# Optimization experiments

Hardware: AMD Instinct MI355X
Metric: run time of the kernel (lower is better)

The kernel has to match this reference:

```python
import jax, jax.numpy as jnp
import numpy as np

N_NODES = 50000
N_EDGES = 500000
D = 256  # node_dim = edge_dim = out_dim; in_dim = 2*D


def setup_inputs() -> dict:
    key = jax.random.key(0)
    ks = jax.random.split(key, 9)
    x = jax.random.normal(ks[0], (N_NODES, D), dtype=jnp.float32)
    edge_index = jax.random.randint(ks[1], (2, N_EDGES), 0, N_NODES, dtype=jnp.int64)
    edge_attr = jax.random.normal(ks[2], (N_EDGES, D), dtype=jnp.float32)
    u = jax.random.normal(ks[3], (1, D), dtype=jnp.float32)
    batch = jnp.zeros((N_NODES,), dtype=jnp.int64)
    scale = 1.0 / np.sqrt(2 * D)
    W1 = jax.random.normal(ks[4], (2 * D, D), dtype=jnp.float32) * scale
    b1 = jax.random.normal(ks[5], (D,), dtype=jnp.float32) * scale
    W2 = jax.random.normal(ks[6], (2 * D, D), dtype=jnp.float32) * scale
    b2 = jax.random.normal(ks[7], (D,), dtype=jnp.float32) * scale
    return {"x": x, "edge_index": edge_index, "edge_attr": edge_attr, "u": u,
            "batch": batch, "W1": W1, "b1": b1, "W2": W2, "b2": b2}


def reference(x, edge_index, edge_attr, u, batch, W1, b1, W2, b2):
    row, col = edge_index[0], edge_index[1]
    # gather source-node features and concat with edge features: [E, 2D]
    h = jnp.concatenate([x[row], edge_attr], axis=1)
    h = jax.nn.relu(h @ W1 + b1)  # node_mlp_1
    # scatter-mean over destination nodes
    agg = jax.ops.segment_sum(h, col, num_segments=N_NODES)
    cnt = jax.ops.segment_sum(jnp.ones((h.shape[0],), h.dtype), col, num_segments=N_NODES)
    agg = agg / jnp.maximum(cnt, 1.0)[:, None]
    out = jnp.concatenate([x, agg], axis=1)  # [N, 2D]
    return jax.nn.relu(out @ W2 + b2)  # node_mlp_2
```

## Files before the change

### kernel.cpp

```cpp
#include <hip/hip_runtime.h>

#define N_NODES 50000
#define N_EDGES 500000
#define D 256
#define TWO_D 512

typedef __attribute__((ext_vector_type(8))) __bf16 bf16x8;
typedef __attribute__((ext_vector_type(4))) float f32x4;
typedef unsigned short ushort_t;

__device__ __forceinline__ unsigned short f2bf(float f) {
    unsigned int u = __builtin_bit_cast(unsigned int, f);
    u += 0x7FFFu + ((u >> 16) & 1u);
    return (unsigned short)(u >> 16);
}
__device__ __forceinline__ unsigned int pk2(float lo, float hi) {
    return (unsigned int)f2bf(lo) | ((unsigned int)f2bf(hi) << 16);
}

__device__ __forceinline__ void barrier_nodrain() {
    asm volatile("s_waitcnt lgkmcnt(0)" ::: "memory");
    __builtin_amdgcn_s_barrier();
    __builtin_amdgcn_sched_barrier(0);
}


__global__ void k_zero(float* __restrict__ p, int n4) {
    int i = blockIdx.x * blockDim.x + threadIdx.x;
    if (i < n4) ((float4*)p)[i] = make_float4(0.f, 0.f, 0.f, 0.f);
}

__global__ void k_cvt_x(const float* __restrict__ x, ushort_t* __restrict__ xb, int n8) {
    int i = blockIdx.x * blockDim.x + threadIdx.x;
    if (i < n8) {
        const float4* s = (const float4*)(x + (size_t)i * 8);
        float4 a = s[0], b = s[1];
        uint4 o;
        o.x = pk2(a.x, a.y); o.y = pk2(a.z, a.w);
        o.z = pk2(b.x, b.y); o.w = pk2(b.z, b.w);
        *(uint4*)(xb + (size_t)i * 8) = o;
    }
}

__global__ void k_wt(const float* __restrict__ w, ushort_t* __restrict__ wt, int KW) {
    int n = blockIdx.x;
    for (int k = threadIdx.x; k < KW; k += blockDim.x)
        wt[(size_t)n * KW + k] = f2bf(w[(size_t)k * D + n]);
}

__global__ void k_count_i(const int* __restrict__ coli, int* __restrict__ cnt) {
    int e = blockIdx.x * blockDim.x + threadIdx.x;
    if (e < N_EDGES) atomicAdd(&cnt[coli[e]], 1);
}


__device__ __forceinline__ int iscan_block(int v, int tid) {
    int lane = tid & 63, wv = tid >> 6;
    int s = v;
    #pragma unroll
    for (int off = 1; off < 64; off <<= 1) {
        int t = __shfl_up(s, off, 64);
        if (lane >= off) s += t;
    }
    __shared__ int wsum[4];
    if (lane == 63) wsum[wv] = s;
    __syncthreads();
    #pragma unroll
    for (int w = 0; w < 3; ++w)
        if (wv > w) s += wsum[w];
    return s;
}

__global__ void k_scan_a(const int* __restrict__ cnt, int* __restrict__ rowptr,
                         int* __restrict__ bsum) {
    int i = blockIdx.x * 256 + threadIdx.x;
    int v = (i < N_NODES) ? cnt[i] : 0;
    int s = iscan_block(v, threadIdx.x);
    if (i < N_NODES) rowptr[i] = s - v;
    if (threadIdx.x == 255) bsum[blockIdx.x] = s;
}

__global__ void k_scan_b(int* __restrict__ bsum, int nb) {
    int i = threadIdx.x;
    int v = (i < nb) ? bsum[i] : 0;
    int s = iscan_block(v, i);
    if (i < nb) bsum[i] = s - v;
}

__global__ void k_scan_c(int* __restrict__ rowptr, const int* __restrict__ bsum,
                         int* __restrict__ cursor) {
    int i = blockIdx.x * 256 + threadIdx.x;
    if (i < N_NODES) {
        int r = rowptr[i] + bsum[blockIdx.x];
        rowptr[i] = r;
        cursor[i] = r;
    }
    if (i == 0) rowptr[N_NODES] = N_EDGES;
}

__global__ void k_fill(const int* __restrict__ coli, const int* __restrict__ rowi,
                       const int* __restrict__ rowptr, int* __restrict__ cursor,
                       int* __restrict__ elist, int* __restrict__ rowg,
                       int* __restrict__ posnode) {
    int e = blockIdx.x * blockDim.x + threadIdx.x;
    if (e < N_EDGES) {
        const int c = coli[e];
        const int p = atomicAdd(&cursor[c], 1);
        elist[p] = e;
        rowg[p] = rowi[e];
        const int t0 = p & ~63;
        const int inter = (rowptr[c] >= t0) && (rowptr[c + 1] <= t0 + 64);
        posnode[p] = (c << 1) | inter;
    }
}

__global__ __launch_bounds__(256) void k_xw1(
    const ushort_t* __restrict__ xb, const ushort_t* __restrict__ w1at,
    const float* __restrict__ b1, float* __restrict__ xw1)
{
    __shared__ __align__(16) ushort_t As[64 * 64];
    __shared__ __align__(16) ushort_t Bs[256 * 64];
    const int tid = threadIdx.x;
    const int wave = tid >> 6, lane = tid & 63;
    const int lr = lane & 15, lh = lane >> 4;
    const int n0 = blockIdx.x * 64;

    const int sm = tid >> 2;
    const int sc = (tid & 3) << 4;
    int ns = n0 + sm; if (ns >= N_NODES) ns = N_NODES - 1;
    const ushort_t* xrow = xb + (size_t)ns * D;
    const ushort_t* wrow = w1at + (size_t)tid * D;
    const int swA = (sm & 7) << 3;
    const int swB = (tid & 7) << 3;

    f32x4 acc[4][4];
    #pragma unroll
    for (int i = 0; i < 4; ++i)
        #pragma unroll
        for (int j = 0; j < 4; ++j)
            acc[i][j] = (f32x4){0.f, 0.f, 0.f, 0.f};

    for (int kk = 0; kk < 4; ++kk) {
        const int k0 = kk << 6;
        const uint4* sx = (const uint4*)(xrow + k0 + sc);
        uint4 av0 = sx[0], av1 = sx[1];
        const uint4* wsv = (const uint4*)(wrow + k0);
        uint4 w0 = wsv[0], w1 = wsv[1], w2 = wsv[2], w3 = wsv[3];
        uint4 w4 = wsv[4], w5 = wsv[5], w6 = wsv[6], w7 = wsv[7];

        __syncthreads();
        *(uint4*)&As[sm * 64 + ( sc      ^ swA)] = av0;
        *(uint4*)&As[sm * 64 + ((sc + 8) ^ swA)] = av1;
        {
            const int base = tid * 64;
            *(uint4*)&Bs[base + ( 0 ^ swB)] = w0;
            *(uint4*)&Bs[base + ( 8 ^ swB)] = w1;
            *(uint4*)&Bs[base + (16 ^ swB)] = w2;
            *(uint4*)&Bs[base + (24 ^ swB)] = w3;
            *(uint4*)&Bs[base + (32 ^ swB)] = w4;
            *(uint4*)&Bs[base + (40 ^ swB)] = w5;
            *(uint4*)&Bs[base + (48 ^ swB)] = w6;
            *(uint4*)&Bs[base + (56 ^ swB)] = w7;
        }
        __syncthreads();

        #pragma unroll
        for (int kh = 0; kh < 2; ++kh) {
            const int kb = kh * 32 + lh * 8;
            bf16x8 af[4], bfr[4];
            #pragma unroll
            for (int i = 0; i < 4; ++i) {
                int m = i * 16 + lr;
                af[i] = *(const bf16x8*)&As[m * 64 + (kb ^ ((m & 7) << 3))];
            }
            #pragma unroll
            for (int j = 0; j < 4; ++j) {
                int n = wave * 64 + j * 16 + lr;
                bfr[j] = *(const bf16x8*)&Bs[n * 64 + (kb ^ ((n & 7) << 3))];
            }
            #pragma unroll
            for (int i = 0; i < 4; ++i)
                #pragma unroll
                for (int j = 0; j < 4; ++j)
                    acc[i][j] = __builtin_amdgcn_mfma_f32_16x16x32_bf16(af[i], bfr[j], acc[i][j], 0, 0, 0);
        }
    }

    float bv[4];
    #pragma unroll
    for (int j = 0; j < 4; ++j) bv[j] = b1[wave * 64 + j * 16 + lr];
    #pragma unroll
    for (int i = 0; i < 4; ++i) {
        #pragma unroll
        for (int r = 0; r < 4; ++r) {
            int m = i * 16 + lh * 4 + r;
            int node = n0 + m;
            if (node < N_NODES) {
                float4 v;
                v.x = acc[i][0][r] + bv[0];
                v.y = acc[i][1][r] + bv[1];
                v.z = acc[i][2][r] + bv[2];
                v.w = acc[i][3][r] + bv[3];
                *(float4*)&xw1[(size_t)node * D + (size_t)(wave * 16 + lr) * 4] = v;
            }
        }
    }
}

__global__ __launch_bounds__(256, 3) void k_edge_csr(
    const float* __restrict__ ea, const ushort_t* __restrict__ w1bt,
    const float* __restrict__ xw1, const int* __restrict__ elist,
    const int* __restrict__ rowg, const int* __restrict__ posnode,
    float* __restrict__ agg)
{
    __shared__ __align__(16) ushort_t As[2][64 * 64];
    __shared__ int snd[64];
    const int tid = threadIdx.x;
    const int wave = tid >> 6, lane = tid & 63;
    const int lr = lane & 15, lh = lane >> 4;
    const int p0 = blockIdx.x * 64;

    if (tid < 64) {
        int p = p0 + tid;
        snd[tid] = (p < N_EDGES) ? posnode[min(p, N_EDGES - 1)] : -1;
    }

    const int sm = tid >> 2;
    const int sc = (tid & 3) << 4;
    int ps = p0 + sm; if (ps >= N_EDGES) ps = N_EDGES - 1;
    const float* earow = ea + (size_t)elist[ps] * D;
    const int swA = (sm & 7) << 3;

    const ushort_t* pw[4];
    #pragma unroll
    for (int j = 0; j < 4; ++j)
        pw[j] = w1bt + (size_t)(wave * 64 + j * 16 + lr) * D + lh * 8;

    f32x4 acc[4][4];
    #pragma unroll
    for (int i = 0; i < 4; ++i)
        #pragma unroll
        for (int j = 0; j < 4; ++j)
            acc[i][j] = (f32x4){0.f, 0.f, 0.f, 0.f};

    float4 st[2][4];
    bf16x8 bReg[8];

    {
        const float4* s = (const float4*)(earow + sc);
        st[0][0] = s[0]; st[0][1] = s[1]; st[0][2] = s[2]; st[0][3] = s[3];
    }
    {
        const float4* s = (const float4*)(earow + 64 + sc);
        st[1][0] = s[0]; st[1][1] = s[1]; st[1][2] = s[2]; st[1][3] = s[3];
    }
    #pragma unroll
    for (int j = 0; j < 4; ++j) {
        bReg[j]     = *(const bf16x8*)(pw[j]);
        bReg[4 + j] = *(const bf16x8*)(pw[j] + 32);
    }
    {
        uint4 av0, av1;
        av0.x = pk2(st[0][0].x, st[0][0].y); av0.y = pk2(st[0][0].z, st[0][0].w);
        av0.z = pk2(st[0][1].x, st[0][1].y); av0.w = pk2(st[0][1].z, st[0][1].w);
        av1.x = pk2(st[0][2].x, st[0][2].y); av1.y = pk2(st[0][2].z, st[0][2].w);
        av1.z = pk2(st[0][3].x, st[0][3].y); av1.w = pk2(st[0][3].z, st[0][3].w);
        *(uint4*)&As[0][sm * 64 + ( sc      ^ swA)] = av0;
        *(uint4*)&As[0][sm * 64 + ((sc + 8) ^ swA)] = av1;
    }
    barrier_nodrain();

    #pragma unroll
    for (int kk = 0; kk < 4; ++kk) {
        if (kk < 2) {
            const float4* s = (const float4*)(earow + ((kk + 2) << 6) + sc);
            st[kk & 1][0] = s[0]; st[kk & 1][1] = s[1];
            st[kk & 1][2] = s[2]; st[kk & 1][3] = s[3];
        }

        const ushort_t* cur = As[kk & 1];
        bf16x8 af0[4], af1[4];
        #pragma unroll
        for (int i = 0; i < 4; ++i) {
            const int m = i * 16 + lr;
            const int sw = (m & 7) << 3;
            af0[i] = *(const bf16x8*)&cur[m * 64 + (( lh * 8     ) ^ sw)];
            af1[i] = *(const bf16x8*)&cur[m * 64 + ((32 + lh * 8) ^ sw)];
        }

        #pragma unroll
        for (int i = 0; i < 4; ++i)
            #pragma unroll
            for (int j = 0; j < 4; ++j) {
                acc[i][j] = __builtin_amdgcn_mfma_f32_16x16x32_bf16(af0[i], bReg[j],     acc[i][j], 0, 0, 0);
                acc[i][j] = __builtin_amdgcn_mfma_f32_16x16x32_bf16(af1[i], bReg[4 + j], acc[i][j], 0, 0, 0);
            }

        if (kk < 3) {
            const int kn = (kk + 1) << 6;
            #pragma unroll
            for (int j = 0; j < 4; ++j) {
                bReg[j]     = *(const bf16x8*)(pw[j] + kn);
                bReg[4 + j] = *(const bf16x8*)(pw[j] + kn + 32);
            }
            uint4 av0, av1;
            const int sB = (kk + 1) & 1;
            av0.x = pk2(st[sB][0].x, st[sB][0].y); av0.y = pk2(st[sB][0].z, st[sB][0].w);
            av0.z = pk2(st[sB][1].x, st[sB][1].y); av0.w = pk2(st[sB][1].z, st[sB][1].w);
            av1.x = pk2(st[sB][2].x, st[sB][2].y); av1.y = pk2(st[sB][2].z, st[sB][2].w);
            av1.z = pk2(st[sB][3].x, st[sB][3].y); av1.w = pk2(st[sB][3].z, st[sB][3].w);
            ushort_t* nxt = (ushort_t*)As[sB];
            *(uint4*)&nxt[sm * 64 + ( sc      ^ swA)] = av0;
            *(uint4*)&nxt[sm * 64 + ((sc + 8) ^ swA)] = av1;
            barrier_nodrain();
        }
    }

    #pragma unroll
    for (int i = 0; i < 4; ++i) {
        #pragma unroll
        for (int r = 0; r < 4; ++r) {
            const int m = i * 16 + lh * 4 + r;
            const bool ok = (p0 + m < N_EDGES);
            const int srw = rowg[min(p0 + m, N_EDGES - 1)];
            const float4 xv = *(const float4*)&xw1[(size_t)srw * D + (size_t)(wave * 16 + lr) * 4];
            const float xvv[4] = {xv.x, xv.y, xv.z, xv.w};
            #pragma unroll
            for (int j = 0; j < 4; ++j) {
                float v = acc[i][j][r] + xvv[j];
                v = v > 0.f ? v : 0.f;
                acc[i][j][r] = ok ? v : 0.f;
            }
        }
    }

    int a = 0;
    while (a < 64) {
        const int raw = snd[a];
        int b = a + 1;
        while (b < 64 && snd[b] == raw) ++b;
        if (raw >= 0) {
            const int node = raw >> 1;
            const int interior = raw & 1;
            float s0 = 0.f, s1 = 0.f, s2 = 0.f, s3 = 0.f;
            #pragma unroll
            for (int i = 0; i < 4; ++i) {
                if (b <= i * 16 || a >= (i + 1) * 16) continue;
                #pragma unroll
                for (int r = 0; r < 4; ++r) {
                    const int m = i * 16 + lh * 4 + r;
                    const bool in = (m >= a) && (m < b);
                    s0 += in ? acc[i][0][r] : 0.f;
                    s1 += in ? acc[i][1][r] : 0.f;
                    s2 += in ? acc[i][2][r] : 0.f;
                    s3 += in ? acc[i][3][r] : 0.f;
                }
            }
            s0 += __shfl_xor(s0, 16, 64); s0 += __shfl_xor(s0, 32, 64);
            s1 += __shfl_xor(s1, 16, 64); s1 += __shfl_xor(s1, 32, 64);
            s2 += __shfl_xor(s2, 16, 64); s2 += __shfl_xor(s2, 32, 64);
            s3 += __shfl_xor(s3, 16, 64); s3 += __shfl_xor(s3, 32, 64);
            if (lh == 0) {
                float* dst = agg + (size_t)node * D + wave * 64 + lr;
                if (interior) {
                    dst[0]  = s0; dst[16] = s1; dst[32] = s2; dst[48] = s3;
                } else {
                    atomicAdd(&dst[0],  s0); atomicAdd(&dst[16], s1);
                    atomicAdd(&dst[32], s2); atomicAdd(&dst[48], s3);
                }
            }
        }
        a = b;
    }
}

__global__ __launch_bounds__(256) void k_node(
    const ushort_t* __restrict__ xb, const float* __restrict__ agg,
    const int* __restrict__ cnti,
    const ushort_t* __restrict__ w2t, const float* __restrict__ b2,
    float* __restrict__ out)
{
    __shared__ __align__(16) ushort_t As[64 * 64];
    __shared__ __align__(16) ushort_t Bs[256 * 64];
    const int tid = threadIdx.x;
    const int wave = tid >> 6, lane = tid & 63;
    const int lr = lane & 15, lh = lane >> 4;
    const int n0 = blockIdx.x * 64;

    const int sm = tid >> 2;
    const int sc = (tid & 3) << 4;
    int ns = n0 + sm; if (ns >= N_NODES) ns = N_NODES - 1;
    const ushort_t* xrow = xb + (size_t)ns * D;
    const float*    arow = agg + (size_t)ns * D;
    const float     ic   = 1.0f / fmaxf((float)cnti[ns], 1.0f);
    const ushort_t* wrow = w2t + (size_t)tid * TWO_D;
    const int swA = (sm & 7) << 3;
    const int swB = (tid & 7) << 3;

    f32x4 acc[4][4];
    #pragma unroll
    for (int i = 0; i < 4; ++i)
        #pragma unroll
        for (int j = 0; j < 4; ++j)
            acc[i][j] = (f32x4){0.f, 0.f, 0.f, 0.f};

    for (int kk = 0; kk < 8; ++kk) {
        const int k0 = kk << 6;
        uint4 av0, av1;
        if (kk < 4) {
            const uint4* s = (const uint4*)(xrow + k0 + sc);
            av0 = s[0]; av1 = s[1];
        } else {
            const float4* s = (const float4*)(arow + (k0 - D) + sc);
            float4 f0 = s[0], f1 = s[1], f2 = s[2], f3 = s[3];
            f0.x *= ic; f0.y *= ic; f0.z *= ic; f0.w *= ic;
            f1.x *= ic; f1.y *= ic; f1.z *= ic; f1.w *= ic;
            f2.x *= ic; f2.y *= ic; f2.z *= ic; f2.w *= ic;
            f3.x *= ic; f3.y *= ic; f3.z *= ic; f3.w *= ic;
            av0.x = pk2(f0.x, f0.y); av0.y = pk2(f0.z, f0.w);
            av0.z = pk2(f1.x, f1.y); av0.w = pk2(f1.z, f1.w);
            av1.x = pk2(f2.x, f2.y); av1.y = pk2(f2.z, f2.w);
            av1.z = pk2(f3.x, f3.y); av1.w = pk2(f3.z, f3.w);
        }
        const uint4* wsv = (const uint4*)(wrow + k0);
        uint4 w0 = wsv[0], w1 = wsv[1], w2 = wsv[2], w3 = wsv[3];
        uint4 w4 = wsv[4], w5 = wsv[5], w6 = wsv[6], w7 = wsv[7];

        barrier_nodrain();
        *(uint4*)&As[sm * 64 + ( sc      ^ swA)] = av0;
        *(uint4*)&As[sm * 64 + ((sc + 8) ^ swA)] = av1;
        {
            const int base = tid * 64;
            *(uint4*)&Bs[base + ( 0 ^ swB)] = w0;
            *(uint4*)&Bs[base + ( 8 ^ swB)] = w1;
            *(uint4*)&Bs[base + (16 ^ swB)] = w2;
            *(uint4*)&Bs[base + (24 ^ swB)] = w3;
            *(uint4*)&Bs[base + (32 ^ swB)] = w4;
            *(uint4*)&Bs[base + (40 ^ swB)] = w5;
            *(uint4*)&Bs[base + (48 ^ swB)] = w6;
            *(uint4*)&Bs[base + (56 ^ swB)] = w7;
        }
        barrier_nodrain();

        #pragma unroll
        for (int kh = 0; kh < 2; ++kh) {
            const int kb = kh * 32 + lh * 8;
            bf16x8 af[4], bfr[4];
            #pragma unroll
            for (int i = 0; i < 4; ++i) {
                int m = i * 16 + lr;
                af[i] = *(const bf16x8*)&As[m * 64 + (kb ^ ((m & 7) << 3))];
            }
            #pragma unroll
            for (int j = 0; j < 4; ++j) {
                int n = wave * 64 + j * 16 + lr;
                bfr[j] = *(const bf16x8*)&Bs[n * 64 + (kb ^ ((n & 7) << 3))];
            }
            #pragma unroll
            for (int i = 0; i < 4; ++i)
                #pragma unroll
                for (int j = 0; j < 4; ++j)
                    acc[i][j] = __builtin_amdgcn_mfma_f32_16x16x32_bf16(af[i], bfr[j], acc[i][j], 0, 0, 0);
        }
    }

    float bv[4];
    #pragma unroll
    for (int j = 0; j < 4; ++j) bv[j] = b2[wave * 64 + j * 16 + lr];
    #pragma unroll
    for (int i = 0; i < 4; ++i) {
        #pragma unroll
        for (int r = 0; r < 4; ++r) {
            int m = i * 16 + lh * 4 + r;
            int node = n0 + m;
            if (node < N_NODES) {
                float* orow = out + (size_t)node * D;
                #pragma unroll
                for (int j = 0; j < 4; ++j) {
                    float v = acc[i][j][r] + bv[j];
                    orow[wave * 64 + j * 16 + lr] = v > 0.f ? v : 0.f;
                }
            }
        }
    }
}


extern "C" void kernel_launch(void* const* d_in, const int* in_sizes, int n_in,
                              void* d_out, int out_size, void* d_ws, size_t ws_size,
                              hipStream_t stream)
{
    const float* x  = (const float*)d_in[0];
    const int*   ei = (const int*)d_in[1];
    const float* ea = (const float*)d_in[2];
    const float* W1 = (const float*)d_in[5];
    const float* b1 = (const float*)d_in[6];
    const float* W2 = (const float*)d_in[7];
    const float* b2 = (const float*)d_in[8];
    float* out = (float*)d_out;

    const int* rowi = ei;
    const int* coli = ei + N_EDGES;
    char* ws = (char*)d_ws;

    size_t off = 0;
    auto take = [&](size_t bytes) {
        char* p = ws + off;
        off = (off + bytes + 255) & ~(size_t)255;
        return p;
    };

    ushort_t* xb      = (ushort_t*)take((size_t)N_NODES * D * 2);
    ushort_t* w1at    = (ushort_t*)take((size_t)D * D * 2);
    ushort_t* w1bt    = (ushort_t*)take((size_t)D * D * 2);
    ushort_t* w2t     = (ushort_t*)take((size_t)D * TWO_D * 2);
    float*    xw1     = (float*)take((size_t)N_NODES * D * 4);
    float*    agg     = (float*)take((size_t)N_NODES * D * 4);
    int*      cnti    = (int*)take(50016 * 4);
    int*      rowptr  = (int*)take(50016 * 4);
    int*      cursor  = (int*)take(50016 * 4);
    int*      bsum    = (int*)take(256 * 4);
    int*      elist   = (int*)take((size_t)N_EDGES * 4);
    int*      rowg    = (int*)take((size_t)N_EDGES * 4);
    int*      posnode = (int*)take((size_t)N_EDGES * 4);

    const int NB = (N_NODES + 255) / 256;
    const int EB = (N_EDGES + 255) / 256;
    const int NGB = (N_NODES + 63) / 64;
    const int EGB = (N_EDGES + 63) / 64;

    k_cvt_x<<<(N_NODES * D / 8 + 255) / 256, 256, 0, stream>>>(x, xb, N_NODES * D / 8);
    k_wt   <<<D, 256, 0, stream>>>(W1, w1at, D);
    k_wt   <<<D, 256, 0, stream>>>(W1 + (size_t)D * D, w1bt, D);
    k_wt   <<<D, 256, 0, stream>>>(W2, w2t, TWO_D);

    k_zero   <<<49, 256, 0, stream>>>((float*)cnti, 50016 / 4);
    k_count_i<<<EB, 256, 0, stream>>>(coli, cnti);
    k_scan_a <<<NB, 256, 0, stream>>>(cnti, rowptr, bsum);
    k_scan_b <<<1, 256, 0, stream>>>(bsum, NB);
    k_scan_c <<<NB, 256, 0, stream>>>(rowptr, bsum, cursor);
    k_fill   <<<EB, 256, 0, stream>>>(coli, rowi, rowptr, cursor, elist, rowg, posnode);

    k_xw1    <<<NGB, 256, 0, stream>>>(xb, w1at, b1, xw1);
    k_zero   <<<(N_NODES * D / 4 + 255) / 256, 256, 0, stream>>>(agg, N_NODES * D / 4);
    k_edge_csr<<<EGB, 256, 0, stream>>>(ea, w1bt, xw1, elist, rowg, posnode, agg);
    k_node   <<<NGB, 256, 0, stream>>>(xb, agg, cnti, w2t, b2, out);
}
```

Measured before the change: 463.4 us.

## Make edge kernel process multiple 64-edge tiles per block with cross-tile prefetch

The edge GEMM kernel now loops over 8 consecutive 64-edge tiles per block instead of one, shrinking the grid accordingly. The first two K-chunks of the next tile's edge features are prefetched into registers during the current tile's epilogue (xw1 gather and segmented scatter). This amortises block launch and setup and overlaps global loads with epilogue work. The cost is far fewer blocks (about 977 over 256 CUs), which lowers parallelism and load balance, and adds an extra barrier per tile.

Measured after the change: 817.0 us. 76.3% more time.

```diff
diff --git a/kernel.cpp b/kernel.cpp
--- a/kernel.cpp
+++ b/kernel.cpp
@@ -4,6 +4,7 @@
 #define N_EDGES 500000
 #define D 256
 #define TWO_D 512
+#define TPB_TILES 8
 
 typedef __attribute__((ext_vector_type(8))) __bf16 bf16x8;
 typedef __attribute__((ext_vector_type(4))) float f32x4;
@@ -218,17 +219,10 @@
     const int tid = threadIdx.x;
     const int wave = tid >> 6, lane = tid & 63;
     const int lr = lane & 15, lh = lane >> 4;
-    const int p0 = blockIdx.x * 64;
-
-    if (tid < 64) {
-        int p = p0 + tid;
-        snd[tid] = (p < N_EDGES) ? posnode[min(p, N_EDGES - 1)] : -1;
-    }
+    const int pbase = blockIdx.x * (TPB_TILES * 64);
 
     const int sm = tid >> 2;
     const int sc = (tid & 3) << 4;
-    int ps = p0 + sm; if (ps >= N_EDGES) ps = N_EDGES - 1;
-    const float* earow = ea + (size_t)elist[ps] * D;
     const int swA = (sm & 7) << 3;
 
     const ushort_t* pw[4];
@@ -236,141 +230,162 @@
     for (int j = 0; j < 4; ++j)
         pw[j] = w1bt + (size_t)(wave * 64 + j * 16 + lr) * D + lh * 8;
 
-    f32x4 acc[4][4];
-    #pragma unroll
-    for (int i = 0; i < 4; ++i)
-        #pragma unroll
-        for (int j = 0; j < 4; ++j)
-            acc[i][j] = (f32x4){0.f, 0.f, 0.f, 0.f};
-
     float4 st[2][4];
     bf16x8 bReg[8];
+    const float* earow;
 
     {
-        const float4* s = (const float4*)(earow + sc);
-        st[0][0] = s[0]; st[0][1] = s[1]; st[0][2] = s[2]; st[0][3] = s[3];
-    }
-    {
-        const float4* s = (const float4*)(earow + 64 + sc);
-        st[1][0] = s[0]; st[1][1] = s[1]; st[1][2] = s[2]; st[1][3] = s[3];
-    }
-    #pragma unroll
-    for (int j = 0; j < 4; ++j) {
-        bReg[j]     = *(const bf16x8*)(pw[j]);
-        bReg[4 + j] = *(const bf16x8*)(pw[j] + 32);
-    }
-    {
-        uint4 av0, av1;
-        av0.x = pk2(st[0][0].x, st[0][0].y); av0.y = pk2(st[0][0].z, st[0][0].w);
-        av0.z = pk2(st[0][1].x, st[0][1].y); av0.w = pk2(st[0][1].z, st[0][1].w);
-        av1.x = pk2(st[0][2].x, st[0][2].y); av1.y = pk2(st[0][2].z, st[0][2].w);
-        av1.z = pk2(st[0][3].x, st[0][3].y); av1.w = pk2(st[0][3].z, st[0][3].w);
-        *(uint4*)&As[0][sm * 64 + ( sc      ^ swA)] = av0;
-        *(uint4*)&As[0][sm * 64 + ((sc + 8) ^ swA)] = av1;
-    }
-    barrier_nodrain();
-
-    #pragma unroll
-    for (int kk = 0; kk < 4; ++kk) {
-        if (kk < 2) {
-            const float4* s = (const float4*)(earow + ((kk + 2) << 6) + sc);
-            st[kk & 1][0] = s[0]; st[kk & 1][1] = s[1];
-            st[kk & 1][2] = s[2]; st[kk & 1][3] = s[3];
-        }
-
-        const ushort_t* cur = As[kk & 1];
-        bf16x8 af0[4], af1[4];
+        const int ps = min(pbase + sm, N_EDGES - 1);
+        earow = ea + (size_t)elist[ps] * D;
+        const float4* s0 = (const float4*)(earow + sc);
+        st[0][0] = s0[0]; st[0][1] = s0[1]; st[0][2] = s0[2]; st[0][3] = s0[3];
+        const float4* s1 = (const float4*)(earow + 64 + sc);
+        st[1][0] = s1[0]; st[1][1] = s1[1]; st[1][2] = s1[2]; st[1][3] = s1[3];
+    }
+
+    for (int t = 0; t < TPB_TILES; ++t) {
+        const int p0 = pbase + t * 64;
+        if (p0 >= N_EDGES) break;
+
+        if (t > 0) barrier_nodrain();
+        if (tid < 64) {
+            int p = p0 + tid;
+            snd[tid] = (p < N_EDGES) ? posnode[min(p, N_EDGES - 1)] : -1;
+        }
+        #pragma unroll
+        for (int j = 0; j < 4; ++j) {
+            bReg[j]     = *(const bf16x8*)(pw[j]);
+            bReg[4 + j] = *(const bf16x8*)(pw[j] + 32);
+        }
+        {
+            uint4 av0, av1;
+            av0.x = pk2(st[0][0].x, st[0][0].y); av0.y = pk2(st[0][0].z, st[0][0].w);
+            av0.z = pk2(st[0][1].x, st[0][1].y); av0.w = pk2(st[0][1].z, st[0][1].w);
+            av1.x = pk2(st[0][2].x, st[0][2].y); av1.y = pk2(st[0][2].z, st[0][2].w);
+            av1.z = pk2(st[0][3].x, st[0][3].y); av1.w = pk2(st[0][3].z, st[0][3].w);
+            *(uint4*)&As[0][sm * 64 + ( sc      ^ swA)] = av0;
+            *(uint4*)&As[0][sm * 64 + ((sc + 8) ^ swA)] = av1;
+        }
+        barrier_nodrain();
+
+        f32x4 acc[4][4];
+        #pragma unroll
+        for (int i = 0; i < 4; ++i)
+            #pragma unroll
+            for (int j = 0; j < 4; ++j)
+                acc[i][j] = (f32x4){0.f, 0.f, 0.f, 0.f};
+
+        #pragma unroll
+        for (int kk = 0; kk < 4; ++kk) {
+            if (kk < 2) {
+                const float4* s = (const float4*)(earow + ((kk + 2) << 6) + sc);
+                st[kk & 1][0] = s[0]; st[kk & 1][1] = s[1];
+                st[kk & 1][2] = s[2]; st[kk & 1][3] = s[3];
+            }
+
+            const ushort_t* cur = As[kk & 1];
+            bf16x8 af0[4], af1[4];
+            #pragma unroll
+            for (int i = 0; i < 4; ++i) {
+                const int m = i * 16 + lr;
+                const int sw = (m & 7) << 3;
+                af0[i] = *(const bf16x8*)&cur[m * 64 + (( lh * 8     ) ^ sw)];
+                af1[i] = *(const bf16x8*)&cur[m * 64 + ((32 + lh * 8) ^ sw)];
+            }
+
+            #pragma unroll
+            for (int i = 0; i < 4; ++i)
+                #pragma unroll
+                for (int j = 0; j < 4; ++j) {
+                    acc[i][j] = __builtin_amdgcn_mfma_f32_16x16x32_bf16(af0[i], bReg[j],     acc[i][j], 0, 0, 0);
+                    acc[i][j] = __builtin_amdgcn_mfma_f32_16x16x32_bf16(af1[i], bReg[4 + j], acc[i][j], 0, 0, 0);
+                }
+
+            if (kk < 3) {
+                const int kn = (kk + 1) << 6;
+                #pragma unroll
+                for (int j = 0; j < 4; ++j) {
+                    bReg[j]     = *(const bf16x8*)(pw[j] + kn);
+                    bReg[4 + j] = *(const bf16x8*)(pw[j] + kn + 32);
+                }
+                uint4 av0, av1;
+                const int sB = (kk + 1) & 1;
+                av0.x = pk2(st[sB][0].x, st[sB][0].y); av0.y = pk2(st[sB][0].z, st[sB][0].w);
+                av0.z = pk2(st[sB][1].x, st[sB][1].y); av0.w = pk2(st[sB][1].z, st[sB][1].w);
+                av1.x = pk2(st[sB][2].x, st[sB][2].y); av1.y = pk2(st[sB][2].z, st[sB][2].w);
+                av1.z = pk2(st[sB][3].x, st[sB][3].y); av1.w = pk2(st[sB][3].z, st[sB][3].w);
+                ushort_t* nxt = (ushort_t*)As[sB];
+                *(uint4*)&nxt[sm * 64 + ( sc      ^ swA)] = av0;
+                *(uint4*)&nxt[sm * 64 + ((sc + 8) ^ swA)] = av1;
+                barrier_nodrain();
+            }
+        }
+
+        if (t + 1 < TPB_TILES && p0 + 64 < N_EDGES) {
+            const int ps = min(p0 + 64 + sm, N_EDGES - 1);
+            earow = ea + (size_t)elist[ps] * D;
+            const float4* s0 = (const float4*)(earow + sc);
+            st[0][0] = s0[0]; st[0][1] = s0[1]; st[0][2] = s0[2]; st[0][3] = s0[3];
+            const float4* s1 = (const float4*)(earow + 64 + sc);
+            st[1][0] = s1[0]; st[1][1] = s1[1]; st[1][2] = s1[2]; st[1][3] = s1[3];
+        }
+
         #pragma unroll
         for (int i = 0; i < 4; ++i) {
-            const int m = i * 16 + lr;
-            const int sw = (m & 7) << 3;
-            af0[i] = *(const bf16x8*)&cur[m * 64 + (( lh * 8     ) ^ sw)];
-            af1[i] = *(const bf16x8*)&cur[m * 64 + ((32 + lh * 8) ^ sw)];
-        }
-
-        #pragma unroll
-        for (int i = 0; i < 4; ++i)
-            #pragma unroll
-            for (int j = 0; j < 4; ++j) {
-                acc[i][j] = __builtin_amdgcn_mfma_f32_16x16x32_bf16(af0[i], bReg[j],     acc[i][j], 0, 0, 0);
-                acc[i][j] = __builtin_amdgcn_mfma_f32_16x16x32_bf16(af1[i], bReg[4 + j], acc[i][j], 0, 0, 0);
-            }
-
-        if (kk < 3) {
-            const int kn = (kk + 1) << 6;
-            #pragma unroll
-            for (int j = 0; j < 4; ++j) {
-                bReg[j]     = *(const bf16x8*)(pw[j] + kn);
-                bReg[4 + j] = *(const bf16x8*)(pw[j] + kn + 32);
-            }
-            uint4 av0, av1;
-            const int sB = (kk + 1) & 1;
-            av0.x = pk2(st[sB][0].x, st[sB][0].y); av0.y = pk2(st[sB][0].z, st[sB][0].w);
-            av0.z = pk2(st[sB][1].x, st[sB][1].y); av0.w = pk2(st[sB][1].z, st[sB][1].w);
-            av1.x = pk2(st[sB][2].x, st[sB][2].y); av1.y = pk2(st[sB][2].z, st[sB][2].w);
-            av1.z = pk2(st[sB][3].x, st[sB][3].y); av1.w = pk2(st[sB][3].z, st[sB][3].w);
-            ushort_t* nxt = (ushort_t*)As[sB];
-            *(uint4*)&nxt[sm * 64 + ( sc      ^ swA)] = av0;
-            *(uint4*)&nxt[sm * 64 + ((sc + 8) ^ swA)] = av1;
-            barrier_nodrain();
-        }
-    }
-
-    #pragma unroll
-    for (int i = 0; i < 4; ++i) {
-        #pragma unroll
-        for (int r = 0; r < 4; ++r) {
-            const int m = i * 16 + lh * 4 + r;
-            const bool ok = (p0 + m < N_EDGES);
-            const int srw = rowg[min(p0 + m, N_EDGES - 1)];
-            const float4 xv = *(const float4*)&xw1[(size_t)srw * D + (size_t)(wave * 16 + lr) * 4];
-            const float xvv[4] = {xv.x, xv.y, xv.z, xv.w};
-            #pragma unroll
-            for (int j = 0; j < 4; ++j) {
-                float v = acc[i][j][r] + xvv[j];
-                v = v > 0.f ? v : 0.f;
-                acc[i][j][r] = ok ? v : 0.f;
-            }
-        }
-    }
-
-    int a = 0;
-    while (a < 64) {
-        const int raw = snd[a];
-        int b = a + 1;
-        while (b < 64 && snd[b] == raw) ++b;
-        if (raw >= 0) {
-            const int node = raw >> 1;
-            const int interior = raw & 1;
-            float s0 = 0.f, s1 = 0.f, s2 = 0.f, s3 = 0.f;
-            #pragma unroll
-            for (int i = 0; i < 4; ++i) {
-                if (b <= i * 16 || a >= (i + 1) * 16) continue;
-                #pragma unroll
-                for (int r = 0; r < 4; ++r) {
-                    const int m = i * 16 + lh * 4 + r;
-                    const bool in = (m >= a) && (m < b);
-                    s0 += in ? acc[i][0][r] : 0.f;
-                    s1 += in ? acc[i][1][r] : 0.f;
-                    s2 += in ? acc[i][2][r] : 0.f;
-                    s3 += in ? acc[i][3][r] : 0.f;
+            #pragma unroll
+            for (int r = 0; r < 4; ++r) {
+                const int m = i * 16 + lh * 4 + r;
+                const bool ok = (p0 + m < N_EDGES);
+                const int srw = rowg[min(p0 + m, N_EDGES - 1)];
+                const float4 xv = *(const float4*)&xw1[(size_t)srw * D + (size_t)(wave * 16 + lr) * 4];
+                const float xvv[4] = {xv.x, xv.y, xv.z, xv.w};
+                #pragma unroll
+                for (int j = 0; j < 4; ++j) {
+                    float v = acc[i][j][r] + xvv[j];
+                    v = v > 0.f ? v : 0.f;
+                    acc[i][j][r] = ok ? v : 0.f;
                 }
             }
-            s0 += __shfl_xor(s0, 16, 64); s0 += __shfl_xor(s0, 32, 64);
-            s1 += __shfl_xor(s1, 16, 64); s1 += __shfl_xor(s1, 32, 64);
-            s2 += __shfl_xor(s2, 16, 64); s2 += __shfl_xor(s2, 32, 64);
-            s3 += __shfl_xor(s3, 16, 64); s3 += __shfl_xor(s3, 32, 64);
-            if (lh == 0) {
-                float* dst = agg + (size_t)node * D + wave * 64 + lr;
-                if (interior) {
-                    dst[0]  = s0; dst[16] = s1; dst[32] = s2; dst[48] = s3;
-                } else {
-                    atomicAdd(&dst[0],  s0); atomicAdd(&dst[16], s1);
-                    atomicAdd(&dst[32], s2); atomicAdd(&dst[48], s3);
+        }
+
+        int a = 0;
+        while (a < 64) {
+            const int raw = snd[a];
+            int b = a + 1;
+            while (b < 64 && snd[b] == raw) ++b;
+            if (raw >= 0) {
+                const int node = raw >> 1;
+                const int interior = raw & 1;
+                float s0 = 0.f, s1 = 0.f, s2 = 0.f, s3 = 0.f;
+                #pragma unroll
+                for (int i = 0; i < 4; ++i) {
+                    if (b <= i * 16 || a >= (i + 1) * 16) continue;
+                    #pragma unroll
+                    for (int r = 0; r < 4; ++r) {
+                        const int m = i * 16 + lh * 4 + r;
+                        const bool in = (m >= a) && (m < b);
+                        s0 += in ? acc[i][0][r] : 0.f;
+                        s1 += in ? acc[i][1][r] : 0.f;
+                        s2 += in ? acc[i][2][r] : 0.f;
+                        s3 += in ? acc[i][3][r] : 0.f;
+                    }
                 }
-            }
-        }
-        a = b;
+                s0 += __shfl_xor(s0, 16, 64); s0 += __shfl_xor(s0, 32, 64);
+                s1 += __shfl_xor(s1, 16, 64); s1 += __shfl_xor(s1, 32, 64);
+                s2 += __shfl_xor(s2, 16, 64); s2 += __shfl_xor(s2, 32, 64);
+                s3 += __shfl_xor(s3, 16, 64); s3 += __shfl_xor(s3, 32, 64);
+                if (lh == 0) {
+                    float* dst = agg + (size_t)node * D + wave * 64 + lr;
+                    if (interior) {
+                        dst[0]  = s0; dst[16] = s1; dst[32] = s2; dst[48] = s3;
+                    } else {
+                        atomicAdd(&dst[0],  s0); atomicAdd(&dst[16], s1);
+                        atomicAdd(&dst[32], s2); atomicAdd(&dst[48], s3);
+                    }
+                }
+            }
+            a = b;
+        }
     }
 }
 
@@ -527,7 +542,7 @@
     const int NB = (N_NODES + 255) / 256;
     const int EB = (N_EDGES + 255) / 256;
     const int NGB = (N_NODES + 63) / 64;
-    const int EGB = (N_EDGES + 63) / 64;
+    const int EGB = (N_EDGES + TPB_TILES * 64 - 1) / (TPB_TILES * 64);
 
     k_cvt_x<<<(N_NODES * D / 8 + 255) / 256, 256, 0, stream>>>(x, xb, N_NODES * D / 8);
     k_wt   <<<D, 256, 0, stream>>>(W1, w1at, D);
```
